# Kernel tuning notes

Measured on AMD Instinct MI355X. Metric: run time of the kernel, lower is better.

Reference implementation:

```python
import jax, jax.numpy as jnp
import numpy as np

N = 50000      # nodes
E = 800000     # edges
P = 100000     # pos/neg candidate edges
IN = 128       # input feat dim
H, D = 2, 64   # heads, out_feats per head
HD = H * D     # 128
NEG_SLOPE = 0.2


def setup_inputs() -> dict:
    key = jax.random.key(0)
    ks = jax.random.split(key, 18)
    def gn(k, shape, fan_in):
        return jax.random.normal(k, shape, jnp.float32) * (1.0 / np.sqrt(fan_in))
    return {
        "x": jax.random.normal(ks[0], (N, IN), jnp.float32),
        "src": jax.random.randint(ks[1], (E,), 0, N),
        "dst": jax.random.randint(ks[2], (E,), 0, N),
        "pos_src": jax.random.randint(ks[3], (P,), 0, N),
        "pos_dst": jax.random.randint(ks[4], (P,), 0, N),
        "neg_src": jax.random.randint(ks[5], (P,), 0, N),
        "neg_dst": jax.random.randint(ks[6], (P,), 0, N),
        "W0": gn(ks[7], (IN, HD), IN),
        "attn0": gn(ks[8], (H, D), D),
        "W1": gn(ks[9], (HD, HD), HD),
        "attn1": gn(ks[10], (H, D), D),
        "Wp1": gn(ks[11], (HD, D), HD),
        "bp1": jnp.zeros((D,), jnp.float32),
        "Wp2": gn(ks[12], (D, D), D),
        "bp2": jnp.zeros((D,), jnp.float32),
        "Wp3": gn(ks[13], (D, 1), D),
        "bp3": jnp.zeros((1,), jnp.float32),
    }


def gatv2_layer(h, W, attn, src, dst, residual):
    # DGL GATv2Conv, share_weights=True, bias=False, feat_drop=attn_drop=0
    feat = (h @ W).reshape(N, H, D)            # [N,H,D]
    el = feat[src]                              # [E,H,D] gather at src
    er = feat[dst]                              # [E,H,D] gather at dst
    e = jax.nn.leaky_relu(el + er, NEG_SLOPE)   # [E,H,D]
    score = jnp.einsum('ehd,hd->eh', e, attn)   # [E,H]
    # edge softmax over incoming edges of each dst node
    m = jax.ops.segment_max(score, dst, num_segments=N)      # [N,H]
    p = jnp.exp(score - m[dst])                               # [E,H]
    s = jax.ops.segment_sum(p, dst, num_segments=N)           # [N,H]
    a = p / s[dst]                                             # [E,H]
    rst = jax.ops.segment_sum(el * a[:, :, None], dst, num_segments=N)  # [N,H,D]
    if residual:
        rst = rst + h.reshape(N, H, D)          # identity res_fc (dims match)
    return jax.nn.elu(rst).reshape(N, HD)       # flatten(1)


def reference(x, src, dst, pos_src, pos_dst, neg_src, neg_dst,
              W0, attn0, W1, attn1, Wp1, bp1, Wp2, bp2, Wp3, bp3):
    h = gatv2_layer(x, W0, attn0, src, dst, residual=False)
    h = gatv2_layer(h, W1, attn1, src, dst, residual=True)

    def predictor(z):
        z = jax.nn.relu(z @ Wp1 + bp1)
        z = jax.nn.relu(z @ Wp2 + bp2)
        return z @ Wp3 + bp3

    h_pos = predictor(h[pos_src] * h[pos_dst])  # [P,1]
    h_neg = predictor(h[neg_src] * h[neg_dst])  # [P,1]
    return (h_pos, h_neg)
```

## Files before the change

kernel.cpp:

```cpp
#include <hip/hip_runtime.h>
#include <math.h>

#define NN 50000
#define NE 800000
#define NP 100000
#define NEG_SLOPE 0.2f
#define SCAN_NB 196
#define LOG2E 1.4426950408889634f

__device__ __forceinline__ float row_sum16(float v) {
    int x = __float_as_int(v);
    v += __int_as_float(__builtin_amdgcn_update_dpp(0, x, 0x128, 0xF, 0xF, true));
    x = __float_as_int(v);
    v += __int_as_float(__builtin_amdgcn_update_dpp(0, x, 0x124, 0xF, 0xF, true));
    x = __float_as_int(v);
    v += __int_as_float(__builtin_amdgcn_update_dpp(0, x, 0x4E, 0xF, 0xF, true));
    x = __float_as_int(v);
    v += __int_as_float(__builtin_amdgcn_update_dpp(0, x, 0xB1, 0xF, 0xF, true));
    return v;
}


__global__ void count_deg(const int* __restrict__ dst, int* __restrict__ cnt) {
    int i = blockIdx.x * blockDim.x + threadIdx.x;
    int st = gridDim.x * blockDim.x;
    const int4* d4 = (const int4*)dst;
    for (; i < NE / 4; i += st) {
        int4 d = d4[i];
        atomicAdd(&cnt[d.x], 1);
        atomicAdd(&cnt[d.y], 1);
        atomicAdd(&cnt[d.z], 1);
        atomicAdd(&cnt[d.w], 1);
    }
}

__global__ __launch_bounds__(256) void scan_part(const int* __restrict__ cnt,
                                                 int* __restrict__ partial) {
    __shared__ int ws[4];
    int t = threadIdx.x;
    int idx = blockIdx.x * 256 + t;
    int v = (idx < NN) ? cnt[idx] : 0;
    #pragma unroll
    for (int mm = 1; mm < 64; mm <<= 1) v += __shfl_xor(v, mm, 64);
    if ((t & 63) == 0) ws[t >> 6] = v;
    __syncthreads();
    if (t == 0) partial[blockIdx.x] = ws[0] + ws[1] + ws[2] + ws[3];
}

__global__ __launch_bounds__(256) void scan_top(const int* __restrict__ partial,
                                                int* __restrict__ partoff,
                                                int* __restrict__ rowptr) {
    __shared__ int wsum[4];
    int t = threadIdx.x, lane = t & 63, w = t >> 6;
    int v = (t < SCAN_NB) ? partial[t] : 0;
    int x = v;
    #pragma unroll
    for (int mm = 1; mm < 64; mm <<= 1) {
        int y = __shfl_up(x, mm, 64);
        if (lane >= mm) x += y;
    }
    if (lane == 63) wsum[w] = x;
    __syncthreads();
    int off = 0;
    for (int k = 0; k < w; ++k) off += wsum[k];
    int excl = off + x - v;
    if (t < SCAN_NB) partoff[t] = excl;
    if (t == SCAN_NB - 1) rowptr[NN] = excl + v;
}

__global__ __launch_bounds__(256) void scan_apply(const int* __restrict__ cnt,
                                                  const int* __restrict__ partoff,
                                                  int* __restrict__ rowptr,
                                                  int* __restrict__ cursor) {
    __shared__ int wsum[4];
    int t = threadIdx.x, lane = t & 63, w = t >> 6;
    int idx = blockIdx.x * 256 + t;
    int v = (idx < NN) ? cnt[idx] : 0;
    int x = v;
    #pragma unroll
    for (int mm = 1; mm < 64; mm <<= 1) {
        int y = __shfl_up(x, mm, 64);
        if (lane >= mm) x += y;
    }
    if (lane == 63) wsum[w] = x;
    __syncthreads();
    int off = partoff[blockIdx.x];
    for (int k = 0; k < w; ++k) off += wsum[k];
    int excl = off + x - v;
    if (idx < NN) { rowptr[idx] = excl; cursor[idx] = excl; }
}

__global__ void scatter_edges(const int* __restrict__ src, const int* __restrict__ dst,
                              int* __restrict__ cursor, int* __restrict__ csrc) {
    int i = blockIdx.x * blockDim.x + threadIdx.x;
    int st = gridDim.x * blockDim.x;
    const int4* s4 = (const int4*)src;
    const int4* d4 = (const int4*)dst;
    for (; i < NE / 4; i += st) {
        int4 s = s4[i];
        int4 d = d4[i];
        int p;
        p = atomicAdd(&cursor[d.x], 1); csrc[p] = s.x;
        p = atomicAdd(&cursor[d.y], 1); csrc[p] = s.y;
        p = atomicAdd(&cursor[d.z], 1); csrc[p] = s.z;
        p = atomicAdd(&cursor[d.w], 1); csrc[p] = s.w;
    }
}


__global__ __launch_bounds__(256) void gemm128(const float* __restrict__ A,
                                               const float* __restrict__ W,
                                               float* __restrict__ out, int nrows) {
    __shared__ float Wt[128 * 132];
    __shared__ float rb[16 * 132];
    int tid = threadIdx.x;
    for (int idx = tid; idx < 128 * 128; idx += 256) {
        int k = idx >> 7, j = idx & 127;
        Wt[j * 132 + k] = W[idx];
    }
    __syncthreads();
    int lane = tid & 63, w = tid >> 6;
    int ntiles = (nrows + 15) >> 4;
    const float* w0p = &Wt[lane * 132];
    const float* w1p = &Wt[(64 + lane) * 132];
    for (int t = blockIdx.x; t < ntiles; t += gridDim.x) {
        int r0 = t << 4;
        for (int i = tid; i < 512; i += 256) {
            int rr = r0 + (i >> 5);
            float4 v = {0.f, 0.f, 0.f, 0.f};
            if (rr < nrows) v = ((const float4*)A)[(size_t)rr * 32 + (i & 31)];
            *(float4*)&rb[(i >> 5) * 132 + (i & 31) * 4] = v;
        }
        __syncthreads();
        float acc[4][2] = {};
        #pragma unroll 4
        for (int k4 = 0; k4 < 32; ++k4) {
            float4 wv0 = *(const float4*)&w0p[k4 * 4];
            float4 wv1 = *(const float4*)&w1p[k4 * 4];
            #pragma unroll
            for (int i2 = 0; i2 < 4; ++i2) {
                float4 av = *(const float4*)&rb[(w * 4 + i2) * 132 + k4 * 4];
                acc[i2][0] = fmaf(av.x, wv0.x, acc[i2][0]);
                acc[i2][0] = fmaf(av.y, wv0.y, acc[i2][0]);
                acc[i2][0] = fmaf(av.z, wv0.z, acc[i2][0]);
                acc[i2][0] = fmaf(av.w, wv0.w, acc[i2][0]);
                acc[i2][1] = fmaf(av.x, wv1.x, acc[i2][1]);
                acc[i2][1] = fmaf(av.y, wv1.y, acc[i2][1]);
                acc[i2][1] = fmaf(av.z, wv1.z, acc[i2][1]);
                acc[i2][1] = fmaf(av.w, wv1.w, acc[i2][1]);
            }
        }
        #pragma unroll
        for (int i2 = 0; i2 < 4; ++i2) {
            int rr = r0 + w * 4 + i2;
            if (rr < nrows) {
                out[(size_t)rr * 128 + lane]      = acc[i2][0];
                out[(size_t)rr * 128 + 64 + lane] = acc[i2][1];
            }
        }
        __syncthreads();
    }
}


#define GAT_EDGE(fv) do {                                          \
    float ex = fv.x + fd.x; ex = fmaxf(ex, NEG_SLOPE * ex);        \
    float ey = fv.y + fd.y; ey = fmaxf(ey, NEG_SLOPE * ey);        \
    float ez = fv.z + fd.z; ez = fmaxf(ez, NEG_SLOPE * ez);        \
    float ew = fv.w + fd.w; ew = fmaxf(ew, NEG_SLOPE * ew);        \
    float part = ex * at.x + ey * at.y + ez * at.z + ew * at.w;    \
    part = row_sum16(part);                                        \
    float p = exp2f(part - m);                                     \
    s += p;                                                        \
    ax = fmaf(fv.x, p, ax);                                        \
    ay = fmaf(fv.y, p, ay);                                        \
    az = fmaf(fv.z, p, az);                                        \
    aw = fmaf(fv.w, p, aw);                                        \
} while (0)

__global__ void gat_fused(const float* __restrict__ feat,
                          const int* __restrict__ rowptr,
                          const int* __restrict__ csrc,
                          const float* __restrict__ attn,
                          const float* __restrict__ resid,
                          float* __restrict__ out) {
    int tid = blockIdx.x * blockDim.x + threadIdx.x;
    int hw = tid >> 5;
    int nhw = (gridDim.x * blockDim.x) >> 5;
    int q = threadIdx.x & 31;
    const float4* feat4 = (const float4*)feat;
    float4 at = ((const float4*)attn)[q];
    at.x *= LOG2E; at.y *= LOG2E; at.z *= LOG2E; at.w *= LOG2E;
    for (int d = hw; d < NN; d += nhw) {
        int beg = rowptr[d], end = rowptr[d + 1];
        float4 fd = feat4[(size_t)d * 32 + q];
        float m = 0.f, s = 0.f;
        float ax = 0.f, ay = 0.f, az = 0.f, aw = 0.f;
        int i = beg;
        float4 f0 = {0.f,0.f,0.f,0.f}, f1 = {0.f,0.f,0.f,0.f}, f2 = {0.f,0.f,0.f,0.f};
        int s3 = 0;
        if (i < end) {
            int p0 = csrc[i];
            int p1 = (i + 1 < end) ? csrc[i + 1] : 0;
            int p2 = (i + 2 < end) ? csrc[i + 2] : 0;
            int p3 = (i + 3 < end) ? csrc[i + 3] : 0;
            s3     = (i + 4 < end) ? csrc[i + 4] : 0;
            float4 fp = feat4[(size_t)p0 * 32 + q];
            if (i + 1 < end) f0 = feat4[(size_t)p1 * 32 + q];
            if (i + 2 < end) f1 = feat4[(size_t)p2 * 32 + q];
            if (i + 3 < end) f2 = feat4[(size_t)p3 * 32 + q];
            float ex = fp.x + fd.x; ex = fmaxf(ex, NEG_SLOPE * ex);
            float ey = fp.y + fd.y; ey = fmaxf(ey, NEG_SLOPE * ey);
            float ez = fp.z + fd.z; ez = fmaxf(ez, NEG_SLOPE * ez);
            float ew = fp.w + fd.w; ew = fmaxf(ew, NEG_SLOPE * ew);
            float part = ex * at.x + ey * at.y + ez * at.z + ew * at.w;
            m = row_sum16(part);
            s = 1.f;
            ax = fp.x; ay = fp.y; az = fp.z; aw = fp.w;
            ++i;
        }
        while (i + 8 <= end) {
            int s4 = csrc[i + 4];
            int s5 = csrc[i + 5];
            int s6 = csrc[i + 6];
            int s7 = csrc[i + 7];
            float4 f3 = feat4[(size_t)s3 * 32 + q];
            GAT_EDGE(f0);
            f0 = feat4[(size_t)s4 * 32 + q];
            GAT_EDGE(f1);
            f1 = feat4[(size_t)s5 * 32 + q];
            GAT_EDGE(f2);
            f2 = feat4[(size_t)s6 * 32 + q];
            GAT_EDGE(f3);
            s3 = s7;
            i += 4;
        }
        while (i < end) {
            float4 f3 = {0.f, 0.f, 0.f, 0.f};
            if (i + 3 < end) f3 = feat4[(size_t)s3 * 32 + q];
            int s4 = (i + 4 < end) ? csrc[i + 4] : 0;
            GAT_EDGE(f0);
            f0 = f1; f1 = f2; f2 = f3; s3 = s4; ++i;
        }
        float inv = s > 0.f ? 1.f / s : 0.f;
        float vx = ax * inv;
        float vy = ay * inv;
        float vz = az * inv;
        float vw = aw * inv;
        if (resid) {
            float4 r = ((const float4*)resid)[(size_t)d * 32 + q];
            vx += r.x; vy += r.y; vz += r.z; vw += r.w;
        }
        vx = vx > 0.f ? vx : expm1f(vx);
        vy = vy > 0.f ? vy : expm1f(vy);
        vz = vz > 0.f ? vz : expm1f(vz);
        vw = vw > 0.f ? vw : expm1f(vw);
        float4 o; o.x = vx; o.y = vy; o.z = vz; o.w = vw;
        ((float4*)out)[(size_t)d * 32 + q] = o;
    }
}


__global__ __launch_bounds__(512, 1) void predictor(const float* __restrict__ h,
                          const int* __restrict__ ps, const int* __restrict__ pd,
                          const int* __restrict__ ns, const int* __restrict__ nd,
                          const float* __restrict__ Wp1, const float* __restrict__ bp1,
                          const float* __restrict__ Wp2, const float* __restrict__ bp2,
                          const float* __restrict__ Wp3, const float* __restrict__ bp3,
                          float* __restrict__ out) {
    __shared__ float S[29696];
    int tid = threadIdx.x;
    for (int idx = tid; idx < 128 * 64; idx += 512) {
        int k = idx >> 6, c = idx & 63;
        S[c * 132 + k] = Wp1[idx];
    }
    for (int idx = tid; idx < 64 * 64; idx += 512) {
        int k = idx >> 6, c = idx & 63;
        S[8448 + c * 68 + k] = Wp2[idx];
    }
    __syncthreads();
    int lane = tid & 63;
    int w = tid >> 6;
    int cg = lane & 15, rg = lane >> 4;
    float* zz = S + 12800 + w * 2112;
    float b1v[4], b2v[4], w3v[4];
    #pragma unroll
    for (int i = 0; i < 4; ++i) {
        b1v[i] = bp1[cg + 16 * i];
        b2v[i] = bp2[cg + 16 * i];
        w3v[i] = Wp3[cg + 16 * i];
    }
    float b3 = bp3[0];
    int gw = blockIdx.x * 8 + w;
    int gnw = gridDim.x * 8;
    int ge = lane >> 2, gp = lane & 3;
    const float4* h4 = (const float4*)h;
    const int NT = (2 * NP) / 16;
    for (int T = gw; T < NT; T += gnw) {
        int e = T * 16 + ge;
        int a, b;
        if (e < NP) { a = ps[e]; b = pd[e]; }
        else        { a = ns[e - NP]; b = nd[e - NP]; }
        const float4* pa = h4 + (size_t)a * 32 + gp;
        const float4* pb = h4 + (size_t)b * 32 + gp;
        #pragma unroll
        for (int qq = 0; qq < 8; ++qq) {
            float4 va = pa[qq * 4];
            float4 vb = pb[qq * 4];
            float4 vz;
            vz.x = va.x * vb.x; vz.y = va.y * vb.y;
            vz.z = va.z * vb.z; vz.w = va.w * vb.w;
            *(float4*)&zz[ge * 132 + gp * 4 + qq * 16] = vz;
        }
        float acc[4][4] = {};
        #pragma unroll 4
        for (int k4 = 0; k4 < 32; ++k4) {
            float4 wv[4], zv[4];
            #pragma unroll
            for (int i = 0; i < 4; ++i)
                wv[i] = *(const float4*)&S[(cg + 16 * i) * 132 + k4 * 4];
            #pragma unroll
            for (int j = 0; j < 4; ++j)
                zv[j] = *(const float4*)&zz[(rg * 4 + j) * 132 + k4 * 4];
            #pragma unroll
            for (int j = 0; j < 4; ++j) {
                #pragma unroll
                for (int i = 0; i < 4; ++i) {
                    acc[j][i] = fmaf(zv[j].x, wv[i].x, acc[j][i]);
                    acc[j][i] = fmaf(zv[j].y, wv[i].y, acc[j][i]);
                    acc[j][i] = fmaf(zv[j].z, wv[i].z, acc[j][i]);
                    acc[j][i] = fmaf(zv[j].w, wv[i].w, acc[j][i]);
                }
            }
        }
        #pragma unroll
        for (int j = 0; j < 4; ++j) {
            #pragma unroll
            for (int i = 0; i < 4; ++i)
                zz[(rg * 4 + j) * 68 + cg + 16 * i] = fmaxf(acc[j][i] + b1v[i], 0.f);
        }
        float acc2[4][4] = {};
        #pragma unroll 4
        for (int k4 = 0; k4 < 16; ++k4) {
            float4 wv[4], zv[4];
            #pragma unroll
            for (int i = 0; i < 4; ++i)
                wv[i] = *(const float4*)&S[8448 + (cg + 16 * i) * 68 + k4 * 4];
            #pragma unroll
            for (int j = 0; j < 4; ++j)
                zv[j] = *(const float4*)&zz[(rg * 4 + j) * 68 + k4 * 4];
            #pragma unroll
            for (int j = 0; j < 4; ++j) {
                #pragma unroll
                for (int i = 0; i < 4; ++i) {
                    acc2[j][i] = fmaf(zv[j].x, wv[i].x, acc2[j][i]);
                    acc2[j][i] = fmaf(zv[j].y, wv[i].y, acc2[j][i]);
                    acc2[j][i] = fmaf(zv[j].z, wv[i].z, acc2[j][i]);
                    acc2[j][i] = fmaf(zv[j].w, wv[i].w, acc2[j][i]);
                }
            }
        }
        float v[4];
        #pragma unroll
        for (int j = 0; j < 4; ++j) {
            float sv = 0.f;
            #pragma unroll
            for (int i = 0; i < 4; ++i)
                sv = fmaf(fmaxf(acc2[j][i] + b2v[i], 0.f), w3v[i], sv);
            v[j] = row_sum16(sv);
        }
        if (cg == 0) {
            float4 o;
            o.x = v[0] + b3; o.y = v[1] + b3; o.z = v[2] + b3; o.w = v[3] + b3;
            *(float4*)&out[T * 16 + rg * 4] = o;
        }
    }
}

extern "C" void kernel_launch(void* const* d_in, const int* in_sizes, int n_in,
                              void* d_out, int out_size, void* d_ws, size_t ws_size,
                              hipStream_t stream) {
    const float* x       = (const float*)d_in[0];
    const int*   src     = (const int*)d_in[1];
    const int*   dst     = (const int*)d_in[2];
    const int*   pos_src = (const int*)d_in[3];
    const int*   pos_dst = (const int*)d_in[4];
    const int*   neg_src = (const int*)d_in[5];
    const int*   neg_dst = (const int*)d_in[6];
    const float* W0      = (const float*)d_in[7];
    const float* attn0   = (const float*)d_in[8];
    const float* W1      = (const float*)d_in[9];
    const float* attn1   = (const float*)d_in[10];
    const float* Wp1     = (const float*)d_in[11];
    const float* bp1     = (const float*)d_in[12];
    const float* Wp2     = (const float*)d_in[13];
    const float* bp2     = (const float*)d_in[14];
    const float* Wp3     = (const float*)d_in[15];
    const float* bp3     = (const float*)d_in[16];

    float* A = (float*)d_ws;
    float* B = A + (size_t)NN * 128;
    float* C = B + (size_t)NN * 128;
    int* cnt     = (int*)(C + (size_t)NN * 128);
    int* rowptr  = cnt + NN;
    int* cursor  = rowptr + NN + 1;
    int* csrc    = cursor + NN;
    int* partial = csrc + NE;
    int* partoff = partial + SCAN_NB;
    float* out = (float*)d_out;

    hipMemsetAsync(cnt, 0, NN * sizeof(int), stream);
    count_deg<<<782, 256, 0, stream>>>(dst, cnt);
    scan_part<<<SCAN_NB, 256, 0, stream>>>(cnt, partial);
    scan_top<<<1, 256, 0, stream>>>(partial, partoff, rowptr);
    scan_apply<<<SCAN_NB, 256, 0, stream>>>(cnt, partoff, rowptr, cursor);
    scatter_edges<<<782, 256, 0, stream>>>(src, dst, cursor, csrc);

    gemm128<<<1024, 256, 0, stream>>>(x, W0, A, NN);
    gat_fused<<<6250, 256, 0, stream>>>(A, rowptr, csrc, attn0, nullptr, C);

    gemm128<<<1024, 256, 0, stream>>>(C, W1, A, NN);
    gat_fused<<<6250, 256, 0, stream>>>(A, rowptr, csrc, attn1, C, B);

    predictor<<<256, 512, 0, stream>>>(B, pos_src, pos_dst, neg_src, neg_dst,
                                       Wp1, bp1, Wp2, bp2, Wp3, bp3, out);
}
```

Before: 389.5 us.

## Fuse CSR construction into a single cooperative kernel with grid syncs

The memset, degree count, three-stage scan and edge scatter are merged into one cooperative kernel of 256 blocks. Grid-wide syncs separate the phases, and the block-offset scan is computed redundantly by each block from the partial sums. This removes several kernel launches and the gaps between them. In exchange it adds grid-sync costs and runs the atomic phases with fewer blocks than before.

```diff
diff --git a/kernel.cpp b/kernel.cpp
--- a/kernel.cpp
+++ b/kernel.cpp
@@ -1,11 +1,13 @@
 #include <hip/hip_runtime.h>
+#include <hip/hip_cooperative_groups.h>
 #include <math.h>
+
+namespace cg = cooperative_groups;
 
 #define NN 50000
 #define NE 800000
 #define NP 100000
 #define NEG_SLOPE 0.2f
-#define SCAN_NB 196
 #define LOG2E 1.4426950408889634f
 
 __device__ __forceinline__ float row_sum16(float v) {
@@ -21,84 +23,60 @@
 }
 
 
-__global__ void count_deg(const int* __restrict__ dst, int* __restrict__ cnt) {
-    int i = blockIdx.x * blockDim.x + threadIdx.x;
-    int st = gridDim.x * blockDim.x;
-    const int4* d4 = (const int4*)dst;
-    for (; i < NE / 4; i += st) {
-        int4 d = d4[i];
+__global__ __launch_bounds__(256) void build_csr(const int* __restrict__ src,
+                                                 const int* __restrict__ dst,
+                                                 int* __restrict__ cnt,
+                                                 int* __restrict__ rowptr,
+                                                 int* __restrict__ cursor,
+                                                 int* __restrict__ csrc,
+                                                 int* __restrict__ partial) {
+    cg::grid_group grid = cg::this_grid();
+    __shared__ int sh[4];
+    int t = threadIdx.x, lane = t & 63, w = t >> 6;
+    int tid = blockIdx.x * 256 + t;
+    int nt = gridDim.x * 256;
+    for (int i = tid; i < NN; i += nt) cnt[i] = 0;
+    grid.sync();
+    const int4* d4v = (const int4*)dst;
+    for (int i = tid; i < NE / 4; i += nt) {
+        int4 d = d4v[i];
         atomicAdd(&cnt[d.x], 1);
         atomicAdd(&cnt[d.y], 1);
         atomicAdd(&cnt[d.z], 1);
         atomicAdd(&cnt[d.w], 1);
     }
-}
-
-__global__ __launch_bounds__(256) void scan_part(const int* __restrict__ cnt,
-                                                 int* __restrict__ partial) {
-    __shared__ int ws[4];
-    int t = threadIdx.x;
-    int idx = blockIdx.x * 256 + t;
-    int v = (idx < NN) ? cnt[idx] : 0;
-    #pragma unroll
-    for (int mm = 1; mm < 64; mm <<= 1) v += __shfl_xor(v, mm, 64);
-    if ((t & 63) == 0) ws[t >> 6] = v;
-    __syncthreads();
-    if (t == 0) partial[blockIdx.x] = ws[0] + ws[1] + ws[2] + ws[3];
-}
-
-__global__ __launch_bounds__(256) void scan_top(const int* __restrict__ partial,
-                                                int* __restrict__ partoff,
-                                                int* __restrict__ rowptr) {
-    __shared__ int wsum[4];
-    int t = threadIdx.x, lane = t & 63, w = t >> 6;
-    int v = (t < SCAN_NB) ? partial[t] : 0;
+    grid.sync();
+    int v = (tid < NN) ? cnt[tid] : 0;
     int x = v;
     #pragma unroll
     for (int mm = 1; mm < 64; mm <<= 1) {
         int y = __shfl_up(x, mm, 64);
         if (lane >= mm) x += y;
     }
-    if (lane == 63) wsum[w] = x;
+    if (lane == 63) sh[w] = x;
     __syncthreads();
-    int off = 0;
-    for (int k = 0; k < w; ++k) off += wsum[k];
-    int excl = off + x - v;
-    if (t < SCAN_NB) partoff[t] = excl;
-    if (t == SCAN_NB - 1) rowptr[NN] = excl + v;
-}
-
-__global__ __launch_bounds__(256) void scan_apply(const int* __restrict__ cnt,
-                                                  const int* __restrict__ partoff,
-                                                  int* __restrict__ rowptr,
-                                                  int* __restrict__ cursor) {
-    __shared__ int wsum[4];
-    int t = threadIdx.x, lane = t & 63, w = t >> 6;
-    int idx = blockIdx.x * 256 + t;
-    int v = (idx < NN) ? cnt[idx] : 0;
-    int x = v;
+    int woff = 0;
+    for (int k = 0; k < w; ++k) woff += sh[k];
+    int myexcl = woff + x - v;
+    if (t == 0) partial[blockIdx.x] = sh[0] + sh[1] + sh[2] + sh[3];
+    __syncthreads();
+    grid.sync();
+    int pv = (t < (int)blockIdx.x) ? partial[t] : 0;
     #pragma unroll
-    for (int mm = 1; mm < 64; mm <<= 1) {
-        int y = __shfl_up(x, mm, 64);
-        if (lane >= mm) x += y;
-    }
-    if (lane == 63) wsum[w] = x;
+    for (int mm = 1; mm < 64; mm <<= 1) pv += __shfl_xor(pv, mm, 64);
+    if (lane == 0) sh[w] = pv;
     __syncthreads();
-    int off = partoff[blockIdx.x];
-    for (int k = 0; k < w; ++k) off += wsum[k];
-    int excl = off + x - v;
-    if (idx < NN) { rowptr[idx] = excl; cursor[idx] = excl; }
-}
-
-__global__ void scatter_edges(const int* __restrict__ src, const int* __restrict__ dst,
-                              int* __restrict__ cursor, int* __restrict__ csrc) {
-    int i = blockIdx.x * blockDim.x + threadIdx.x;
-    int st = gridDim.x * blockDim.x;
-    const int4* s4 = (const int4*)src;
-    const int4* d4 = (const int4*)dst;
-    for (; i < NE / 4; i += st) {
-        int4 s = s4[i];
-        int4 d = d4[i];
+    int blockoff = sh[0] + sh[1] + sh[2] + sh[3];
+    if (tid < NN) {
+        rowptr[tid] = blockoff + myexcl;
+        cursor[tid] = blockoff + myexcl;
+    }
+    if (tid == NN - 1) rowptr[NN] = blockoff + myexcl + v;
+    grid.sync();
+    const int4* s4v = (const int4*)src;
+    for (int i = tid; i < NE / 4; i += nt) {
+        int4 s = s4v[i];
+        int4 d = d4v[i];
         int p;
         p = atomicAdd(&cursor[d.x], 1); csrc[p] = s.x;
         p = atomicAdd(&cursor[d.y], 1); csrc[p] = s.y;
@@ -406,15 +384,14 @@
     int* cursor  = rowptr + NN + 1;
     int* csrc    = cursor + NN;
     int* partial = csrc + NE;
-    int* partoff = partial + SCAN_NB;
     float* out = (float*)d_out;
 
-    hipMemsetAsync(cnt, 0, NN * sizeof(int), stream);
-    count_deg<<<782, 256, 0, stream>>>(dst, cnt);
-    scan_part<<<SCAN_NB, 256, 0, stream>>>(cnt, partial);
-    scan_top<<<1, 256, 0, stream>>>(partial, partoff, rowptr);
-    scan_apply<<<SCAN_NB, 256, 0, stream>>>(cnt, partoff, rowptr, cursor);
-    scatter_edges<<<782, 256, 0, stream>>>(src, dst, cursor, csrc);
+    {
+        void* args[] = {(void*)&src, (void*)&dst, (void*)&cnt, (void*)&rowptr,
+                        (void*)&cursor, (void*)&csrc, (void*)&partial};
+        hipLaunchCooperativeKernel((void*)build_csr, dim3(256), dim3(256),
+                                   args, 0, stream);
+    }
 
     gemm128<<<1024, 256, 0, stream>>>(x, W0, A, NN);
     gat_fused<<<6250, 256, 0, stream>>>(A, rowptr, csrc, attn0, nullptr, C);
```

After: 497.6 us. 1.28x slower.

## Fuse degree count into first GEMM launch and drop scan_top kernel

Applied to the files above, without the earlier changes.

Merges the degree-counting atomics into the first feature GEMM launch by giving extra blocks the counting work, so the two independent tasks run concurrently in one grid. Removes the single-block scan_top kernel by having each scan_apply block reduce the preceding partial sums itself. This cuts two kernel launches and serializations. The trade-off is redundant partial-sum reads per scan block, plus GEMM blocks now sharing the device with atomic-heavy count blocks.

```diff
diff --git a/kernel.cpp b/kernel.cpp
--- a/kernel.cpp
+++ b/kernel.cpp
@@ -7,6 +7,8 @@
 #define NEG_SLOPE 0.2f
 #define SCAN_NB 196
 #define LOG2E 1.4426950408889634f
+#define GEMM_BLOCKS 1024
+#define COUNT_BLOCKS 782
 
 __device__ __forceinline__ float row_sum16(float v) {
     int x = __float_as_int(v);
@@ -21,18 +23,88 @@
 }
 
 
-__global__ void count_deg(const int* __restrict__ dst, int* __restrict__ cnt) {
-    int i = blockIdx.x * blockDim.x + threadIdx.x;
-    int st = gridDim.x * blockDim.x;
-    const int4* d4 = (const int4*)dst;
-    for (; i < NE / 4; i += st) {
-        int4 d = d4[i];
-        atomicAdd(&cnt[d.x], 1);
-        atomicAdd(&cnt[d.y], 1);
-        atomicAdd(&cnt[d.z], 1);
-        atomicAdd(&cnt[d.w], 1);
-    }
-}
+__device__ __forceinline__ void gemm_body(const float* __restrict__ A,
+                                          const float* __restrict__ W,
+                                          float* __restrict__ out, int nrows,
+                                          int gemm_blocks) {
+    __shared__ float Wt[128 * 132];
+    __shared__ float rb[16 * 132];
+    int tid = threadIdx.x;
+    for (int idx = tid; idx < 128 * 128; idx += 256) {
+        int k = idx >> 7, j = idx & 127;
+        Wt[j * 132 + k] = W[idx];
+    }
+    __syncthreads();
+    int lane = tid & 63, w = tid >> 6;
+    int ntiles = (nrows + 15) >> 4;
+    const float* w0p = &Wt[lane * 132];
+    const float* w1p = &Wt[(64 + lane) * 132];
+    for (int t = blockIdx.x; t < ntiles; t += gemm_blocks) {
+        int r0 = t << 4;
+        for (int i = tid; i < 512; i += 256) {
+            int rr = r0 + (i >> 5);
+            float4 v = {0.f, 0.f, 0.f, 0.f};
+            if (rr < nrows) v = ((const float4*)A)[(size_t)rr * 32 + (i & 31)];
+            *(float4*)&rb[(i >> 5) * 132 + (i & 31) * 4] = v;
+        }
+        __syncthreads();
+        float acc[4][2] = {};
+        #pragma unroll 4
+        for (int k4 = 0; k4 < 32; ++k4) {
+            float4 wv0 = *(const float4*)&w0p[k4 * 4];
+            float4 wv1 = *(const float4*)&w1p[k4 * 4];
+            #pragma unroll
+            for (int i2 = 0; i2 < 4; ++i2) {
+                float4 av = *(const float4*)&rb[(w * 4 + i2) * 132 + k4 * 4];
+                acc[i2][0] = fmaf(av.x, wv0.x, acc[i2][0]);
+                acc[i2][0] = fmaf(av.y, wv0.y, acc[i2][0]);
+                acc[i2][0] = fmaf(av.z, wv0.z, acc[i2][0]);
+                acc[i2][0] = fmaf(av.w, wv0.w, acc[i2][0]);
+                acc[i2][1] = fmaf(av.x, wv1.x, acc[i2][1]);
+                acc[i2][1] = fmaf(av.y, wv1.y, acc[i2][1]);
+                acc[i2][1] = fmaf(av.z, wv1.z, acc[i2][1]);
+                acc[i2][1] = fmaf(av.w, wv1.w, acc[i2][1]);
+            }
+        }
+        #pragma unroll
+        for (int i2 = 0; i2 < 4; ++i2) {
+            int rr = r0 + w * 4 + i2;
+            if (rr < nrows) {
+                out[(size_t)rr * 128 + lane]      = acc[i2][0];
+                out[(size_t)rr * 128 + 64 + lane] = acc[i2][1];
+            }
+        }
+        __syncthreads();
+    }
+}
+
+__global__ __launch_bounds__(256) void gemm128(const float* __restrict__ A,
+                                               const float* __restrict__ W,
+                                               float* __restrict__ out, int nrows) {
+    gemm_body(A, W, out, nrows, gridDim.x);
+}
+
+__global__ __launch_bounds__(256) void gemm128_count(const float* __restrict__ A,
+                                                     const float* __restrict__ W,
+                                                     float* __restrict__ out, int nrows,
+                                                     const int* __restrict__ dst,
+                                                     int* __restrict__ cnt) {
+    if (blockIdx.x < GEMM_BLOCKS) {
+        gemm_body(A, W, out, nrows, GEMM_BLOCKS);
+    } else {
+        int i = (blockIdx.x - GEMM_BLOCKS) * 256 + threadIdx.x;
+        int st = COUNT_BLOCKS * 256;
+        const int4* d4 = (const int4*)dst;
+        for (; i < NE / 4; i += st) {
+            int4 d = d4[i];
+            atomicAdd(&cnt[d.x], 1);
+            atomicAdd(&cnt[d.y], 1);
+            atomicAdd(&cnt[d.z], 1);
+            atomicAdd(&cnt[d.w], 1);
+        }
+    }
+}
+
 
 __global__ __launch_bounds__(256) void scan_part(const int* __restrict__ cnt,
                                                  int* __restrict__ partial) {
@@ -47,33 +119,17 @@
     if (t == 0) partial[blockIdx.x] = ws[0] + ws[1] + ws[2] + ws[3];
 }
 
-__global__ __launch_bounds__(256) void scan_top(const int* __restrict__ partial,
-                                                int* __restrict__ partoff,
-                                                int* __restrict__ rowptr) {
-    __shared__ int wsum[4];
-    int t = threadIdx.x, lane = t & 63, w = t >> 6;
-    int v = (t < SCAN_NB) ? partial[t] : 0;
-    int x = v;
-    #pragma unroll
-    for (int mm = 1; mm < 64; mm <<= 1) {
-        int y = __shfl_up(x, mm, 64);
-        if (lane >= mm) x += y;
-    }
-    if (lane == 63) wsum[w] = x;
-    __syncthreads();
-    int off = 0;
-    for (int k = 0; k < w; ++k) off += wsum[k];
-    int excl = off + x - v;
-    if (t < SCAN_NB) partoff[t] = excl;
-    if (t == SCAN_NB - 1) rowptr[NN] = excl + v;
-}
-
 __global__ __launch_bounds__(256) void scan_apply(const int* __restrict__ cnt,
-                                                  const int* __restrict__ partoff,
+                                                  const int* __restrict__ partial,
                                                   int* __restrict__ rowptr,
                                                   int* __restrict__ cursor) {
-    __shared__ int wsum[4];
+    __shared__ int sh[4];
+    __shared__ int shb[4];
     int t = threadIdx.x, lane = t & 63, w = t >> 6;
+    int pv = (t < (int)blockIdx.x) ? partial[t] : 0;
+    #pragma unroll
+    for (int mm = 1; mm < 64; mm <<= 1) pv += __shfl_xor(pv, mm, 64);
+    if (lane == 0) shb[w] = pv;
     int idx = blockIdx.x * 256 + t;
     int v = (idx < NN) ? cnt[idx] : 0;
     int x = v;
@@ -82,12 +138,13 @@
         int y = __shfl_up(x, mm, 64);
         if (lane >= mm) x += y;
     }
-    if (lane == 63) wsum[w] = x;
+    if (lane == 63) sh[w] = x;
     __syncthreads();
-    int off = partoff[blockIdx.x];
-    for (int k = 0; k < w; ++k) off += wsum[k];
+    int off = shb[0] + shb[1] + shb[2] + shb[3];
+    for (int k = 0; k < w; ++k) off += sh[k];
     int excl = off + x - v;
     if (idx < NN) { rowptr[idx] = excl; cursor[idx] = excl; }
+    if (idx == NN - 1) rowptr[NN] = excl + v;
 }
 
 __global__ void scatter_edges(const int* __restrict__ src, const int* __restrict__ dst,
@@ -104,61 +161,6 @@
         p = atomicAdd(&cursor[d.y], 1); csrc[p] = s.y;
         p = atomicAdd(&cursor[d.z], 1); csrc[p] = s.z;
         p = atomicAdd(&cursor[d.w], 1); csrc[p] = s.w;
-    }
-}
-
-
-__global__ __launch_bounds__(256) void gemm128(const float* __restrict__ A,
-                                               const float* __restrict__ W,
-                                               float* __restrict__ out, int nrows) {
-    __shared__ float Wt[128 * 132];
-    __shared__ float rb[16 * 132];
-    int tid = threadIdx.x;
-    for (int idx = tid; idx < 128 * 128; idx += 256) {
-        int k = idx >> 7, j = idx & 127;
-        Wt[j * 132 + k] = W[idx];
-    }
-    __syncthreads();
-    int lane = tid & 63, w = tid >> 6;
-    int ntiles = (nrows + 15) >> 4;
-    const float* w0p = &Wt[lane * 132];
-    const float* w1p = &Wt[(64 + lane) * 132];
-    for (int t = blockIdx.x; t < ntiles; t += gridDim.x) {
-        int r0 = t << 4;
-        for (int i = tid; i < 512; i += 256) {
-            int rr = r0 + (i >> 5);
-            float4 v = {0.f, 0.f, 0.f, 0.f};
-            if (rr < nrows) v = ((const float4*)A)[(size_t)rr * 32 + (i & 31)];
-            *(float4*)&rb[(i >> 5) * 132 + (i & 31) * 4] = v;
-        }
-        __syncthreads();
-        float acc[4][2] = {};
-        #pragma unroll 4
-        for (int k4 = 0; k4 < 32; ++k4) {
-            float4 wv0 = *(const float4*)&w0p[k4 * 4];
-            float4 wv1 = *(const float4*)&w1p[k4 * 4];
-            #pragma unroll
-            for (int i2 = 0; i2 < 4; ++i2) {
-                float4 av = *(const float4*)&rb[(w * 4 + i2) * 132 + k4 * 4];
-                acc[i2][0] = fmaf(av.x, wv0.x, acc[i2][0]);
-                acc[i2][0] = fmaf(av.y, wv0.y, acc[i2][0]);
-                acc[i2][0] = fmaf(av.z, wv0.z, acc[i2][0]);
-                acc[i2][0] = fmaf(av.w, wv0.w, acc[i2][0]);
-                acc[i2][1] = fmaf(av.x, wv1.x, acc[i2][1]);
-                acc[i2][1] = fmaf(av.y, wv1.y, acc[i2][1]);
-                acc[i2][1] = fmaf(av.z, wv1.z, acc[i2][1]);
-                acc[i2][1] = fmaf(av.w, wv1.w, acc[i2][1]);
-            }
-        }
-        #pragma unroll
-        for (int i2 = 0; i2 < 4; ++i2) {
-            int rr = r0 + w * 4 + i2;
-            if (rr < nrows) {
-                out[(size_t)rr * 128 + lane]      = acc[i2][0];
-                out[(size_t)rr * 128 + 64 + lane] = acc[i2][1];
-            }
-        }
-        __syncthreads();
     }
 }
 
@@ -406,17 +408,15 @@
     int* cursor  = rowptr + NN + 1;
     int* csrc    = cursor + NN;
     int* partial = csrc + NE;
-    int* partoff = partial + SCAN_NB;
     float* out = (float*)d_out;
 
     hipMemsetAsync(cnt, 0, NN * sizeof(int), stream);
-    count_deg<<<782, 256, 0, stream>>>(dst, cnt);
+    gemm128_count<<<GEMM_BLOCKS + COUNT_BLOCKS, 256, 0, stream>>>(x, W0, A, NN, dst, cnt);
+
     scan_part<<<SCAN_NB, 256, 0, stream>>>(cnt, partial);
-    scan_top<<<1, 256, 0, stream>>>(partial, partoff, rowptr);
-    scan_apply<<<SCAN_NB, 256, 0, stream>>>(cnt, partoff, rowptr, cursor);
+    scan_apply<<<SCAN_NB, 256, 0, stream>>>(cnt, partial, rowptr, cursor);
     scatter_edges<<<782, 256, 0, stream>>>(src, dst, cursor, csrc);
 
-    gemm128<<<1024, 256, 0, stream>>>(x, W0, A, NN);
     gat_fused<<<6250, 256, 0, stream>>>(A, rowptr, csrc, attn0, nullptr, C);
 
     gemm128<<<1024, 256, 0, stream>>>(C, W1, A, NN);
```

After: 378.5 us. 2.8% less time.
